# Kernel optimization log

Measured on AMD Instinct MI355X. Metric: run time of the kernel, lower is better.

Reference implementation:

```python
import jax, jax.numpy as jnp
import numpy as np

B, T, S, H = 4, 256, 1024, 256


def setup_inputs() -> dict:
    key = jax.random.key(0)
    k1, k2, k3, k4, k5, k6 = jax.random.split(key, 6)
    query = jax.random.normal(k1, (B, T, H), dtype=jnp.float32)
    encoder_outputs = jax.random.normal(k2, (B, S, H), dtype=jnp.float32)
    src_lengths = jax.random.randint(k3, (B,), 1, S + 1).astype(jnp.int64)
    scale = 1.0 / np.sqrt(H)
    W_h = jax.random.normal(k4, (H, H), dtype=jnp.float32) * scale
    W_s = jax.random.normal(k5, (H, H), dtype=jnp.float32) * scale
    v = jax.random.normal(k6, (H,), dtype=jnp.float32) * scale
    return {
        "query": query,
        "encoder_outputs": encoder_outputs,
        "src_lengths": src_lengths,
        "W_h": W_h,
        "W_s": W_s,
        "v": v,
    }


def reference(query, encoder_outputs, src_lengths, W_h, W_s, v):
    # score(h_i, s_j) = v^T tanh(W_h h_i + W_s s_j)
    # project once per sequence, then broadcast-add over (tgt, src)
    q_proj = jnp.einsum("bth,hk->btk", query, W_h)            # (B, T, H)
    e_proj = jnp.einsum("bsh,hk->bsk", encoder_outputs, W_s)  # (B, S, H)
    # (B, T, S, H) additive intermediate -> reduce with v
    feats = jnp.tanh(q_proj[:, :, None, :] + e_proj[:, None, :, :])
    scores = jnp.einsum("btsh,h->bts", feats, v)              # (B, T, S)
    # mask padding positions (src positions >= src_lengths[b])
    valid = jnp.arange(scores.shape[-1])[None, :] < src_lengths[:, None]  # (B, S)
    scores = jnp.where(valid[:, None, :], scores, jnp.finfo(scores.dtype).min)
    attn = jax.nn.softmax(scores, axis=-1)                    # (B, T, S)
    attn_out = jnp.einsum("bts,bsh->bth", attn, encoder_outputs)  # (B, T, H)
    return attn_out
```

## Files before the change

### kernel.cpp

```cpp
#include <hip/hip_runtime.h>
#include <math.h>

#define NB 4
#define NT 256
#define NS 1024
#define NH 256
#define SBK 64
#define NSQ (NS / SBK)
#define WT 4
#define BTR 16
#define BS (NB * NS)

typedef _Float16 half4 __attribute__((ext_vector_type(4)));

static constexpr float CTWO   = 2.8853900817779268f;
static constexpr float LOG2E  = 1.4426950408889634f;
static constexpr float ACLAMP = 62.0f;

__global__ __launch_bounds__(256) void proj_kernel(const float* __restrict__ Q,
                                                   const float* __restrict__ E,
                                                   const float* __restrict__ W_h,
                                                   const float* __restrict__ W_s,
                                                   float* __restrict__ tq,
                                                   float* __restrict__ tet) {
  __shared__ float As[32][68];
  __shared__ float Bs[32][68];
  const int tid = threadIdx.x;
  int r0 = blockIdx.x * 64;
  const int n0 = blockIdx.y * 64;
  const bool is_q = (r0 < NB * NT);
  const float* A;
  const float* W;
  if (is_q) { A = Q; W = W_h; }
  else      { A = E; W = W_s; r0 -= NB * NT; }
  const int tx = tid & 15;
  const int ty = tid >> 4;
  float acc[4][4] = {};
  for (int k0 = 0; k0 < NH; k0 += 32) {
    {
      const int r = tid >> 2;
      const int kq = (tid & 3) * 8;
      const float* src = A + (size_t)(r0 + r) * NH + k0 + kq;
      float4 v0 = *(const float4*)(src);
      float4 v1 = *(const float4*)(src + 4);
      As[kq + 0][r] = v0.x; As[kq + 1][r] = v0.y; As[kq + 2][r] = v0.z; As[kq + 3][r] = v0.w;
      As[kq + 4][r] = v1.x; As[kq + 5][r] = v1.y; As[kq + 6][r] = v1.z; As[kq + 7][r] = v1.w;
    }
    {
      const int k = tid >> 3;
      const int nq = (tid & 7) * 8;
      const float* src = W + (size_t)(k0 + k) * NH + n0 + nq;
      *(float4*)&Bs[k][nq]     = *(const float4*)(src);
      *(float4*)&Bs[k][nq + 4] = *(const float4*)(src + 4);
    }
    __syncthreads();
    #pragma unroll
    for (int k = 0; k < 32; ++k) {
      float4 a = *(const float4*)&As[k][ty * 4];
      float4 b = *(const float4*)&Bs[k][tx * 4];
      const float av[4] = {a.x, a.y, a.z, a.w};
      const float bv[4] = {b.x, b.y, b.z, b.w};
      #pragma unroll
      for (int i = 0; i < 4; ++i)
        #pragma unroll
        for (int j = 0; j < 4; ++j)
          acc[i][j] = fmaf(av[i], bv[j], acc[i][j]);
    }
    __syncthreads();
  }
  #pragma unroll
  for (int i = 0; i < 4; ++i) {
    float vals[4];
    #pragma unroll
    for (int j = 0; j < 4; ++j) {
      float x = acc[i][j] * CTWO;
      x = fminf(fmaxf(x, -ACLAMP), ACLAMP);
      vals[j] = __builtin_amdgcn_exp2f(x);
    }
    const int r = r0 + ty * 4 + i;
    if (is_q) {
      #pragma unroll
      for (int j = 0; j < 4; ++j)
        tq[(size_t)r * NH + n0 + tx * 4 + j] = vals[j];
    } else {
      const int h4 = (n0 >> 2) + tx;
      const int b  = r >> 10;
      const int s  = r & 1023;
      const int sq = s >> 6;
      const int sl = s & 63;
      float4 w = {vals[0], vals[1], vals[2], vals[3]};
      *(float4*)&tet[(((size_t)(b * 16 + sq) * 64 + h4) * 64 + sl) * 4] = w;
    }
  }
}

#define PAIR(qa, ea, va, qb, eb, vb, ACC)                                  \
  {                                                                        \
    float ta = fmaf((qa), (ea), 1.0f);                                     \
    float tb = fmaf((qb), (eb), 1.0f);                                     \
    float num = fmaf((va), tb, (vb) * ta);                                 \
    float den = ta * tb;                                                   \
    ACC = fmaf(num, __builtin_amdgcn_rcpf(den), ACC);                      \
  }

__global__ __launch_bounds__(256) void attn_main_kernel(
    const float4* __restrict__ tqq,
    const float4* __restrict__ tet,
    const float4* __restrict__ enc4,
    const int* __restrict__ src_len,
    const float4* __restrict__ vq,
    half4* __restrict__ poh, float* __restrict__ mbuf, float* __restrict__ lbuf) {
  __shared__ float4 p_lds[4 * SBK];
  const int tid = threadIdx.x;
  const int wid = tid >> 6;
  const int lane = tid & 63;
  const int bx = blockIdx.x;
  const int low6 = bx & 63;
  const int b  = low6 & 3;
  const int sq = ((low6 >> 2) + 4 * b) & 15;
  const int tg = bx >> 6;
  const int btbase = b * NT + tg * BTR;
  const int s0 = sq * SBK;
  const int len = src_len[b];

  if (s0 >= len) {
    if (tid < BTR) {
      mbuf[(size_t)(btbase + tid) * NSQ + sq] = -INFINITY;
      lbuf[(size_t)(btbase + tid) * NSQ + sq] = 0.f;
    }
    return;
  }

  float sumv;
  {
    float4 v4 = vq[lane];
    float sv = (v4.x + v4.y) + (v4.z + v4.w);
    #pragma unroll
    for (int o = 32; o > 0; o >>= 1) sv += __shfl_xor(sv, o, 64);
    sumv = sv;
  }

  const int wrow = btbase + wid * WT;
  const int gs0 = b * NS + s0;
  const bool ok = (s0 + lane) < len;

  float acc[WT] = {0.f, 0.f, 0.f, 0.f};
  const float4* tep = tet + (size_t)(b * 16 + sq) * 64 * 64 + lane;
  const float4* qp  = tqq + (size_t)wrow * 64;
  #pragma unroll 8
  for (int h4 = 0; h4 < 64; ++h4) {
    const float4 e  = tep[h4 * 64];
    const float4 vv = vq[h4];
    #pragma unroll
    for (int t = 0; t < WT; ++t) {
      const float4 q = qp[t * 64 + h4];
      PAIR(q.x, e.x, vv.x, q.y, e.y, vv.y, acc[t]);
      PAIR(q.z, e.z, vv.z, q.w, e.w, vv.w, acc[t]);
    }
  }

  float pv[WT];
  #pragma unroll
  for (int t = 0; t < WT; ++t) {
    float x = ok ? fmaf(-2.f, acc[t], sumv) : -INFINITY;
    float m = x;
    #pragma unroll
    for (int o = 32; o > 0; o >>= 1) m = fmaxf(m, __shfl_xor(m, o, 64));
    float p = __builtin_amdgcn_exp2f((x - m) * LOG2E);
    float l = p;
    #pragma unroll
    for (int o = 32; o > 0; o >>= 1) l += __shfl_xor(l, o, 64);
    pv[t] = p;
    if (lane == 0) {
      mbuf[(size_t)(wrow + t) * NSQ + sq] = m;
      lbuf[(size_t)(wrow + t) * NSQ + sq] = l;
    }
  }
  p_lds[wid * SBK + lane] = make_float4(pv[0], pv[1], pv[2], pv[3]);

  float4 o[WT];
  #pragma unroll
  for (int t = 0; t < WT; ++t) o[t] = make_float4(0.f, 0.f, 0.f, 0.f);
  const float4* ep = enc4 + (size_t)gs0 * 64 + lane;
  #pragma unroll 4
  for (int s = 0; s < SBK; ++s) {
    const float4 e = ep[(size_t)s * 64];
    const float4 p = p_lds[wid * SBK + s];
    o[0].x = fmaf(p.x, e.x, o[0].x); o[0].y = fmaf(p.x, e.y, o[0].y);
    o[0].z = fmaf(p.x, e.z, o[0].z); o[0].w = fmaf(p.x, e.w, o[0].w);
    o[1].x = fmaf(p.y, e.x, o[1].x); o[1].y = fmaf(p.y, e.y, o[1].y);
    o[1].z = fmaf(p.y, e.z, o[1].z); o[1].w = fmaf(p.y, e.w, o[1].w);
    o[2].x = fmaf(p.z, e.x, o[2].x); o[2].y = fmaf(p.z, e.y, o[2].y);
    o[2].z = fmaf(p.z, e.z, o[2].z); o[2].w = fmaf(p.z, e.w, o[2].w);
    o[3].x = fmaf(p.w, e.x, o[3].x); o[3].y = fmaf(p.w, e.y, o[3].y);
    o[3].z = fmaf(p.w, e.z, o[3].z); o[3].w = fmaf(p.w, e.w, o[3].w);
  }
  #pragma unroll
  for (int t = 0; t < WT; ++t) {
    half4 h;
    h.x = (_Float16)o[t].x; h.y = (_Float16)o[t].y;
    h.z = (_Float16)o[t].z; h.w = (_Float16)o[t].w;
    poh[((size_t)(wrow + t) * NSQ + sq) * 64 + lane] = h;
  }
}

__global__ __launch_bounds__(256) void combine_kernel(const half4* __restrict__ poh,
                                                      const float* __restrict__ mbuf,
                                                      const float* __restrict__ lbuf,
                                                      float4* __restrict__ out4) {
  const int bt = blockIdx.x * 4 + (threadIdx.x >> 6);
  const int lane = threadIdx.x & 63;
  float m[NSQ], l[NSQ];
  float M = -INFINITY;
  #pragma unroll
  for (int i = 0; i < NSQ; ++i) {
    m[i] = mbuf[(size_t)bt * NSQ + i];
    l[i] = lbuf[(size_t)bt * NSQ + i];
    M = fmaxf(M, m[i]);
  }
  float L = 0.f;
  float4 o = make_float4(0.f, 0.f, 0.f, 0.f);
  #pragma unroll
  for (int i = 0; i < NSQ; ++i) {
    if (m[i] > -INFINITY) {
      float w = __builtin_amdgcn_exp2f((m[i] - M) * LOG2E);
      L = fmaf(w, l[i], L);
      half4 h = poh[((size_t)bt * NSQ + i) * 64 + lane];
      o.x = fmaf(w, (float)h.x, o.x);
      o.y = fmaf(w, (float)h.y, o.y);
      o.z = fmaf(w, (float)h.z, o.z);
      o.w = fmaf(w, (float)h.w, o.w);
    }
  }
  const float r = __builtin_amdgcn_rcpf(L);
  o.x *= r; o.y *= r; o.z *= r; o.w *= r;
  out4[(size_t)bt * 64 + lane] = o;
}

extern "C" void kernel_launch(void* const* d_in, const int* in_sizes, int n_in,
                              void* d_out, int out_size, void* d_ws, size_t ws_size,
                              hipStream_t stream) {
  const float* query = (const float*)d_in[0];
  const float* enc   = (const float*)d_in[1];
  const int*   slen  = (const int*)d_in[2];
  const float* W_h   = (const float*)d_in[3];
  const float* W_s   = (const float*)d_in[4];
  const float* v     = (const float*)d_in[5];
  float* out = (float*)d_out;

  float* ws = (float*)d_ws;
  float* tq  = ws;
  float* tet = tq + (size_t)NB * NT * NH;
  half4* poh = (half4*)(tet + (size_t)NB * NS * NH);
  float* mb  = (float*)((char*)poh + (size_t)NB * NT * NSQ * NH * 2);
  float* lb  = mb + (size_t)NB * NT * NSQ;

  hipLaunchKernelGGL(proj_kernel, dim3((NB * (NT + NS)) / 64, NH / 64), dim3(256), 0, stream,
                     query, enc, W_h, W_s, tq, tet);
  hipLaunchKernelGGL(attn_main_kernel, dim3(NB * NSQ * (NT / BTR)), dim3(256), 0, stream,
                     (const float4*)tq, (const float4*)tet, (const float4*)enc, slen,
                     (const float4*)v, poh, mb, lb);
  hipLaunchKernelGGL(combine_kernel, dim3(NB * NT / 4), dim3(256), 0, stream,
                     poh, mb, lb, (float4*)out);
}
```

Before: 86.31 us.

## Stage encoder tiles in LDS cooperatively and remap block order by t-group

```diff
diff --git a/kernel.cpp b/kernel.cpp
--- a/kernel.cpp
+++ b/kernel.cpp
@@ -110,15 +110,16 @@
     const int* __restrict__ src_len,
     const float4* __restrict__ vq,
     half4* __restrict__ poh, float* __restrict__ mbuf, float* __restrict__ lbuf) {
+  __shared__ float4 buf[1024];
   __shared__ float4 p_lds[4 * SBK];
   const int tid = threadIdx.x;
   const int wid = tid >> 6;
   const int lane = tid & 63;
   const int bx = blockIdx.x;
-  const int low6 = bx & 63;
-  const int b  = low6 & 3;
-  const int sq = ((low6 >> 2) + 4 * b) & 15;
-  const int tg = bx >> 6;
+  const int tg = bx & 15;
+  const int w  = bx >> 4;
+  const int b  = w & 3;
+  const int sq = ((w >> 2) + 4 * b) & 15;
   const int btbase = b * NT + tg * BTR;
   const int s0 = sq * SBK;
   const int len = src_len[b];
@@ -145,17 +146,27 @@
   const bool ok = (s0 + lane) < len;
 
   float acc[WT] = {0.f, 0.f, 0.f, 0.f};
-  const float4* tep = tet + (size_t)(b * 16 + sq) * 64 * 64 + lane;
+  const float4* wbase = tet + (size_t)(b * 16 + sq) * 4096;
   const float4* qp  = tqq + (size_t)wrow * 64;
-  #pragma unroll 8
-  for (int h4 = 0; h4 < 64; ++h4) {
-    const float4 e  = tep[h4 * 64];
-    const float4 vv = vq[h4];
-    #pragma unroll
-    for (int t = 0; t < WT; ++t) {
-      const float4 q = qp[t * 64 + h4];
-      PAIR(q.x, e.x, vv.x, q.y, e.y, vv.y, acc[t]);
-      PAIR(q.z, e.z, vv.z, q.w, e.w, vv.w, acc[t]);
+  for (int c = 0; c < 4; ++c) {
+    float4 stg[4];
+    #pragma unroll
+    for (int i = 0; i < 4; ++i) stg[i] = wbase[c * 1024 + i * 256 + tid];
+    __syncthreads();
+    #pragma unroll
+    for (int i = 0; i < 4; ++i) buf[i * 256 + tid] = stg[i];
+    __syncthreads();
+    #pragma unroll
+    for (int h4c = 0; h4c < 16; ++h4c) {
+      const int h4 = c * 16 + h4c;
+      const float4 e  = buf[h4c * 64 + lane];
+      const float4 vv = vq[h4];
+      #pragma unroll
+      for (int t = 0; t < WT; ++t) {
+        const float4 q = qp[t * 64 + h4];
+        PAIR(q.x, e.x, vv.x, q.y, e.y, vv.y, acc[t]);
+        PAIR(q.z, e.z, vv.z, q.w, e.w, vv.w, acc[t]);
+      }
     }
   }
 
@@ -181,19 +192,29 @@
   float4 o[WT];
   #pragma unroll
   for (int t = 0; t < WT; ++t) o[t] = make_float4(0.f, 0.f, 0.f, 0.f);
-  const float4* ep = enc4 + (size_t)gs0 * 64 + lane;
-  #pragma unroll 4
-  for (int s = 0; s < SBK; ++s) {
-    const float4 e = ep[(size_t)s * 64];
-    const float4 p = p_lds[wid * SBK + s];
-    o[0].x = fmaf(p.x, e.x, o[0].x); o[0].y = fmaf(p.x, e.y, o[0].y);
-    o[0].z = fmaf(p.x, e.z, o[0].z); o[0].w = fmaf(p.x, e.w, o[0].w);
-    o[1].x = fmaf(p.y, e.x, o[1].x); o[1].y = fmaf(p.y, e.y, o[1].y);
-    o[1].z = fmaf(p.y, e.z, o[1].z); o[1].w = fmaf(p.y, e.w, o[1].w);
-    o[2].x = fmaf(p.z, e.x, o[2].x); o[2].y = fmaf(p.z, e.y, o[2].y);
-    o[2].z = fmaf(p.z, e.z, o[2].z); o[2].w = fmaf(p.z, e.w, o[2].w);
-    o[3].x = fmaf(p.w, e.x, o[3].x); o[3].y = fmaf(p.w, e.y, o[3].y);
-    o[3].z = fmaf(p.w, e.z, o[3].z); o[3].w = fmaf(p.w, e.w, o[3].w);
+  const float4* ebase = enc4 + (size_t)gs0 * 64;
+  for (int c = 0; c < 4; ++c) {
+    float4 stg[4];
+    #pragma unroll
+    for (int i = 0; i < 4; ++i) stg[i] = ebase[c * 1024 + i * 256 + tid];
+    __syncthreads();
+    #pragma unroll
+    for (int i = 0; i < 4; ++i) buf[i * 256 + tid] = stg[i];
+    __syncthreads();
+    #pragma unroll
+    for (int sc = 0; sc < 16; ++sc) {
+      const int s = c * 16 + sc;
+      const float4 e = buf[sc * 64 + lane];
+      const float4 p = p_lds[wid * SBK + s];
+      o[0].x = fmaf(p.x, e.x, o[0].x); o[0].y = fmaf(p.x, e.y, o[0].y);
+      o[0].z = fmaf(p.x, e.z, o[0].z); o[0].w = fmaf(p.x, e.w, o[0].w);
+      o[1].x = fmaf(p.y, e.x, o[1].x); o[1].y = fmaf(p.y, e.y, o[1].y);
+      o[1].z = fmaf(p.y, e.z, o[1].z); o[1].w = fmaf(p.y, e.w, o[1].w);
+      o[2].x = fmaf(p.z, e.x, o[2].x); o[2].y = fmaf(p.z, e.y, o[2].y);
+      o[2].z = fmaf(p.z, e.z, o[2].z); o[2].w = fmaf(p.z, e.w, o[2].w);
+      o[3].x = fmaf(p.w, e.x, o[3].x); o[3].y = fmaf(p.w, e.y, o[3].y);
+      o[3].z = fmaf(p.w, e.z, o[3].z); o[3].w = fmaf(p.w, e.w, o[3].w);
+    }
   }
   #pragma unroll
   for (int t = 0; t < WT; ++t) {
```

Result: slower. 90.58 us (+4.9%).

## Use atomic work-stealing per wave in attention kernel and bound combine by length

Applied to the files above, without the earlier changes.

```diff
diff --git a/kernel.cpp b/kernel.cpp
--- a/kernel.cpp
+++ b/kernel.cpp
@@ -8,7 +8,8 @@
 #define SBK 64
 #define NSQ (NS / SBK)
 #define WT 4
-#define BTR 16
+#define NTQ (NT / WT)
+#define NWORK (NB * NTQ * NSQ)
 #define BS (NB * NS)
 
 typedef _Float16 half4 __attribute__((ext_vector_type(4)));
@@ -109,27 +110,12 @@
     const float4* __restrict__ enc4,
     const int* __restrict__ src_len,
     const float4* __restrict__ vq,
-    half4* __restrict__ poh, float* __restrict__ mbuf, float* __restrict__ lbuf) {
+    half4* __restrict__ poh, float* __restrict__ mbuf, float* __restrict__ lbuf,
+    int* __restrict__ ctr) {
   __shared__ float4 p_lds[4 * SBK];
   const int tid = threadIdx.x;
   const int wid = tid >> 6;
   const int lane = tid & 63;
-  const int bx = blockIdx.x;
-  const int low6 = bx & 63;
-  const int b  = low6 & 3;
-  const int sq = ((low6 >> 2) + 4 * b) & 15;
-  const int tg = bx >> 6;
-  const int btbase = b * NT + tg * BTR;
-  const int s0 = sq * SBK;
-  const int len = src_len[b];
-
-  if (s0 >= len) {
-    if (tid < BTR) {
-      mbuf[(size_t)(btbase + tid) * NSQ + sq] = -INFINITY;
-      lbuf[(size_t)(btbase + tid) * NSQ + sq] = 0.f;
-    }
-    return;
-  }
 
   float sumv;
   {
@@ -140,97 +126,110 @@
     sumv = sv;
   }
 
-  const int wrow = btbase + wid * WT;
-  const int gs0 = b * NS + s0;
-  const bool ok = (s0 + lane) < len;
-
-  float acc[WT] = {0.f, 0.f, 0.f, 0.f};
-  const float4* tep = tet + (size_t)(b * 16 + sq) * 64 * 64 + lane;
-  const float4* qp  = tqq + (size_t)wrow * 64;
-  #pragma unroll 8
-  for (int h4 = 0; h4 < 64; ++h4) {
-    const float4 e  = tep[h4 * 64];
-    const float4 vv = vq[h4];
+  for (;;) {
+    int item = 0;
+    if (lane == 0) item = atomicAdd(ctr, 1);
+    item = __shfl(item, 0, 64);
+    if (item >= NWORK) break;
+
+    const int b  = item >> 10;
+    const int sq = (item >> 6) & 15;
+    const int tquad = item & 63;
+    const int len = src_len[b];
+    const int s0 = sq * SBK;
+    if (s0 >= len) continue;
+
+    const int wrow = b * NT + tquad * WT;
+    const int gs0 = b * NS + s0;
+    const bool ok = (s0 + lane) < len;
+
+    float acc[WT] = {0.f, 0.f, 0.f, 0.f};
+    const float4* tep = tet + (size_t)(b * 16 + sq) * 4096 + lane;
+    const float4* qp  = tqq + (size_t)wrow * 64;
+    #pragma unroll 8
+    for (int h4 = 0; h4 < 64; ++h4) {
+      const float4 e  = tep[h4 * 64];
+      const float4 vv = vq[h4];
+      #pragma unroll
+      for (int t = 0; t < WT; ++t) {
+        const float4 q = qp[t * 64 + h4];
+        PAIR(q.x, e.x, vv.x, q.y, e.y, vv.y, acc[t]);
+        PAIR(q.z, e.z, vv.z, q.w, e.w, vv.w, acc[t]);
+      }
+    }
+
+    float pv[WT];
     #pragma unroll
     for (int t = 0; t < WT; ++t) {
-      const float4 q = qp[t * 64 + h4];
-      PAIR(q.x, e.x, vv.x, q.y, e.y, vv.y, acc[t]);
-      PAIR(q.z, e.z, vv.z, q.w, e.w, vv.w, acc[t]);
-    }
-  }
-
-  float pv[WT];
-  #pragma unroll
-  for (int t = 0; t < WT; ++t) {
-    float x = ok ? fmaf(-2.f, acc[t], sumv) : -INFINITY;
-    float m = x;
-    #pragma unroll
-    for (int o = 32; o > 0; o >>= 1) m = fmaxf(m, __shfl_xor(m, o, 64));
-    float p = __builtin_amdgcn_exp2f((x - m) * LOG2E);
-    float l = p;
-    #pragma unroll
-    for (int o = 32; o > 0; o >>= 1) l += __shfl_xor(l, o, 64);
-    pv[t] = p;
-    if (lane == 0) {
-      mbuf[(size_t)(wrow + t) * NSQ + sq] = m;
-      lbuf[(size_t)(wrow + t) * NSQ + sq] = l;
-    }
-  }
-  p_lds[wid * SBK + lane] = make_float4(pv[0], pv[1], pv[2], pv[3]);
-
-  float4 o[WT];
-  #pragma unroll
-  for (int t = 0; t < WT; ++t) o[t] = make_float4(0.f, 0.f, 0.f, 0.f);
-  const float4* ep = enc4 + (size_t)gs0 * 64 + lane;
-  #pragma unroll 4
-  for (int s = 0; s < SBK; ++s) {
-    const float4 e = ep[(size_t)s * 64];
-    const float4 p = p_lds[wid * SBK + s];
-    o[0].x = fmaf(p.x, e.x, o[0].x); o[0].y = fmaf(p.x, e.y, o[0].y);
-    o[0].z = fmaf(p.x, e.z, o[0].z); o[0].w = fmaf(p.x, e.w, o[0].w);
-    o[1].x = fmaf(p.y, e.x, o[1].x); o[1].y = fmaf(p.y, e.y, o[1].y);
-    o[1].z = fmaf(p.y, e.z, o[1].z); o[1].w = fmaf(p.y, e.w, o[1].w);
-    o[2].x = fmaf(p.z, e.x, o[2].x); o[2].y = fmaf(p.z, e.y, o[2].y);
-    o[2].z = fmaf(p.z, e.z, o[2].z); o[2].w = fmaf(p.z, e.w, o[2].w);
-    o[3].x = fmaf(p.w, e.x, o[3].x); o[3].y = fmaf(p.w, e.y, o[3].y);
-    o[3].z = fmaf(p.w, e.z, o[3].z); o[3].w = fmaf(p.w, e.w, o[3].w);
-  }
-  #pragma unroll
-  for (int t = 0; t < WT; ++t) {
-    half4 h;
-    h.x = (_Float16)o[t].x; h.y = (_Float16)o[t].y;
-    h.z = (_Float16)o[t].z; h.w = (_Float16)o[t].w;
-    poh[((size_t)(wrow + t) * NSQ + sq) * 64 + lane] = h;
+      float x = ok ? fmaf(-2.f, acc[t], sumv) : -INFINITY;
+      float m = x;
+      #pragma unroll
+      for (int o = 32; o > 0; o >>= 1) m = fmaxf(m, __shfl_xor(m, o, 64));
+      float p = __builtin_amdgcn_exp2f((x - m) * LOG2E);
+      float l = p;
+      #pragma unroll
+      for (int o = 32; o > 0; o >>= 1) l += __shfl_xor(l, o, 64);
+      pv[t] = p;
+      if (lane == 0) {
+        mbuf[(size_t)(wrow + t) * NSQ + sq] = m;
+        lbuf[(size_t)(wrow + t) * NSQ + sq] = l;
+      }
+    }
+    p_lds[wid * SBK + lane] = make_float4(pv[0], pv[1], pv[2], pv[3]);
+
+    float4 o[WT];
+    #pragma unroll
+    for (int t = 0; t < WT; ++t) o[t] = make_float4(0.f, 0.f, 0.f, 0.f);
+    const float4* ep = enc4 + (size_t)gs0 * 64 + lane;
+    #pragma unroll 4
+    for (int s = 0; s < SBK; ++s) {
+      const float4 e = ep[(size_t)s * 64];
+      const float4 p = p_lds[wid * SBK + s];
+      o[0].x = fmaf(p.x, e.x, o[0].x); o[0].y = fmaf(p.x, e.y, o[0].y);
+      o[0].z = fmaf(p.x, e.z, o[0].z); o[0].w = fmaf(p.x, e.w, o[0].w);
+      o[1].x = fmaf(p.y, e.x, o[1].x); o[1].y = fmaf(p.y, e.y, o[1].y);
+      o[1].z = fmaf(p.y, e.z, o[1].z); o[1].w = fmaf(p.y, e.w, o[1].w);
+      o[2].x = fmaf(p.z, e.x, o[2].x); o[2].y = fmaf(p.z, e.y, o[2].y);
+      o[2].z = fmaf(p.z, e.z, o[2].z); o[2].w = fmaf(p.z, e.w, o[2].w);
+      o[3].x = fmaf(p.w, e.x, o[3].x); o[3].y = fmaf(p.w, e.y, o[3].y);
+      o[3].z = fmaf(p.w, e.z, o[3].z); o[3].w = fmaf(p.w, e.w, o[3].w);
+    }
+    #pragma unroll
+    for (int t = 0; t < WT; ++t) {
+      half4 h;
+      h.x = (_Float16)o[t].x; h.y = (_Float16)o[t].y;
+      h.z = (_Float16)o[t].z; h.w = (_Float16)o[t].w;
+      poh[((size_t)(wrow + t) * NSQ + sq) * 64 + lane] = h;
+    }
   }
 }
 
 __global__ __launch_bounds__(256) void combine_kernel(const half4* __restrict__ poh,
                                                       const float* __restrict__ mbuf,
                                                       const float* __restrict__ lbuf,
+                                                      const int* __restrict__ src_len,
                                                       float4* __restrict__ out4) {
   const int bt = blockIdx.x * 4 + (threadIdx.x >> 6);
   const int lane = threadIdx.x & 63;
+  const int len = src_len[bt >> 8];
+  const int nvalid = (len + SBK - 1) / SBK;
   float m[NSQ], l[NSQ];
   float M = -INFINITY;
-  #pragma unroll
-  for (int i = 0; i < NSQ; ++i) {
+  for (int i = 0; i < nvalid; ++i) {
     m[i] = mbuf[(size_t)bt * NSQ + i];
     l[i] = lbuf[(size_t)bt * NSQ + i];
     M = fmaxf(M, m[i]);
   }
   float L = 0.f;
   float4 o = make_float4(0.f, 0.f, 0.f, 0.f);
-  #pragma unroll
-  for (int i = 0; i < NSQ; ++i) {
-    if (m[i] > -INFINITY) {
-      float w = __builtin_amdgcn_exp2f((m[i] - M) * LOG2E);
-      L = fmaf(w, l[i], L);
-      half4 h = poh[((size_t)bt * NSQ + i) * 64 + lane];
-      o.x = fmaf(w, (float)h.x, o.x);
-      o.y = fmaf(w, (float)h.y, o.y);
-      o.z = fmaf(w, (float)h.z, o.z);
-      o.w = fmaf(w, (float)h.w, o.w);
-    }
+  for (int i = 0; i < nvalid; ++i) {
+    float w = __builtin_amdgcn_exp2f((m[i] - M) * LOG2E);
+    L = fmaf(w, l[i], L);
+    half4 h = poh[((size_t)bt * NSQ + i) * 64 + lane];
+    o.x = fmaf(w, (float)h.x, o.x);
+    o.y = fmaf(w, (float)h.y, o.y);
+    o.z = fmaf(w, (float)h.z, o.z);
+    o.w = fmaf(w, (float)h.w, o.w);
   }
   const float r = __builtin_amdgcn_rcpf(L);
   o.x *= r; o.y *= r; o.z *= r; o.w *= r;
@@ -254,12 +253,14 @@
   half4* poh = (half4*)(tet + (size_t)NB * NS * NH);
   float* mb  = (float*)((char*)poh + (size_t)NB * NT * NSQ * NH * 2);
   float* lb  = mb + (size_t)NB * NT * NSQ;
-
+  int*   ctr = (int*)(lb + (size_t)NB * NT * NSQ);
+
+  hipMemsetAsync(ctr, 0, sizeof(int), stream);
   hipLaunchKernelGGL(proj_kernel, dim3((NB * (NT + NS)) / 64, NH / 64), dim3(256), 0, stream,
                      query, enc, W_h, W_s, tq, tet);
-  hipLaunchKernelGGL(attn_main_kernel, dim3(NB * NSQ * (NT / BTR)), dim3(256), 0, stream,
+  hipLaunchKernelGGL(attn_main_kernel, dim3(2048), dim3(256), 0, stream,
                      (const float4*)tq, (const float4*)tet, (const float4*)enc, slen,
-                     (const float4*)v, poh, mb, lb);
+                     (const float4*)v, poh, mb, lb, ctr);
   hipLaunchKernelGGL(combine_kernel, dim3(NB * NT / 4), dim3(256), 0, stream,
-                     poh, mb, lb, (float4*)out);
-}
+                     poh, mb, lb, slen, (float4*)out);
+}
```

Result: slower. 207.7 us (+140.7%).
